# Optimization experiments

Hardware: AMD Instinct MI355X
Metric: run time of the kernel (lower is better)

## Reference

```python
import jax, jax.numpy as jnp
import numpy as np

GRID = 0.5
NG = 48
NC = 16  # output channels
CHUNK = 256  # atoms per scan step (bounds peak memory)
E2 = float(np.exp(2.0))
# order matches pro_keys ['O','C','N','S'] with vdw_dic
VDW = jnp.array([1.52, 1.7, 1.55, 1.8], dtype=jnp.float32)


def setup_inputs() -> dict:
    key = jax.random.key(0)
    k1, k2, k3 = jax.random.split(key, 3)
    N = 2048
    coords = jax.random.uniform(k1, (N, 3), dtype=jnp.float32) * (NG * GRID)  # [0, 24)
    ch_idx = jax.random.randint(k2, (N,), 0, 4, dtype=jnp.int32)
    fg = jax.random.randint(k3, (N,), 0, 16, dtype=jnp.int32)
    return {"coords": coords, "ch_idx": ch_idx, "fg": fg}


def _channel_weights(ch_idx, fg):
    # base element channel 0..3
    w = jax.nn.one_hot(ch_idx, NC, dtype=jnp.float32)
    # fg routing: 14 -> +ch4 +ch5; 15 -> +ch6 +ch9; 12/13 -> nothing; else -> +ch(fg+4)
    c1 = jnp.where(fg == 14, 4, jnp.where(fg == 15, 6, fg + 4))
    c1 = jnp.where((fg == 12) | (fg == 13), -1, c1)  # one_hot(-1) == zeros
    c2 = jnp.where(fg == 14, 5, jnp.where(fg == 15, 9, -1))
    return w + jax.nn.one_hot(c1, NC, dtype=jnp.float32) + jax.nn.one_hot(c2, NC, dtype=jnp.float32)


def _grid_forward(coords, r, w):
    # coords [N,3], r [N] vdw radii, w [N,16] channel weights -> [16,48,48,48]
    gx = GRID * jnp.arange(NG, dtype=jnp.float32)  # grid point coordinates
    nchunk = coords.shape[0] // CHUNK
    coords_c = coords.reshape(nchunk, CHUNK, 3)
    r_c = r.reshape(nchunk, CHUNK)
    w_c = w.reshape(nchunk, CHUNK, NC)

    def body(acc, args):
        c, rr, ww = args  # [CHUNK,3], [CHUNK], [CHUNK,16]
        dx2 = (c[:, 0, None] - gx) ** 2  # [CHUNK,48]
        dy2 = (c[:, 1, None] - gx) ** 2
        dz2 = (c[:, 2, None] - gx) ** 2
        d2 = dx2[:, :, None, None] + dy2[:, None, :, None] + dz2[:, None, None, :]  # [CHUNK,48,48,48]
        d = jnp.sqrt(d2)
        r_ = rr[:, None, None, None]
        r2 = r_ * r_
        f1 = jnp.exp(-2.0 * d2 / r2)
        f2 = 4.0 * d2 / (E2 * r2) - 12.0 * d / (E2 * r_) + 9.0 / E2
        val = jnp.where(d < r_, f1, jnp.where(d < 1.5 * r_, f2, 0.0))
        acc = acc + jnp.einsum('nc,nxyz->cxyz', ww, val)
        return acc, None

    out, _ = jax.lax.scan(body, jnp.zeros((NC, NG, NG, NG), jnp.float32), (coords_c, r_c, w_c))
    return out


def reference(coords, ch_idx, fg):
    r = VDW[ch_idx]
    w = _channel_weights(ch_idx, fg)
    return _grid_forward(coords, r, w)
```

## Files before the change

### kernel.cpp

```cpp
#include <hip/hip_runtime.h>

#define NG 48
#define NC 16
#define NPTS (NG * NG * NG)
#define E2F 7.3890561f
#define NINE_OVER_E2 1.2180175f

#define BR 4
#define CAP 128

__device__ __constant__ float c_vdw[4] = {1.52f, 1.7f, 1.55f, 1.8f};

__global__ void prep_kernel(const float* __restrict__ coords,
                            const int* __restrict__ ch_idx,
                            const int* __restrict__ fg,
                            float4* __restrict__ atomA,
                            float4* __restrict__ atomB, int natoms)
{
    const int i = blockIdx.x * blockDim.x + threadIdx.x;
    if (i >= natoms) return;
    const float x = coords[3 * i + 0];
    const float y = coords[3 * i + 1];
    const float z = coords[3 * i + 2];
    const int ci = ch_idx[i];
    const int f  = fg[i];
    const float r  = c_vdw[ci];
    const float r2 = r * r;
    int c1 = (f == 14) ? 4 : ((f == 15) ? 6 : f + 4);
    if (f == 12 || f == 13) c1 = -1;
    const int c2 = (f == 14) ? 5 : ((f == 15) ? 9 : -1);
    int mask = 1 << ci;
    if (c1 >= 0) mask |= 1 << c1;
    if (c2 >= 0) mask |= 1 << c2;
    atomA[i] = make_float4(x, y, z, 1.5f * r);
    atomB[i] = make_float4(-2.0f / r2, 4.0f / (E2F * r2),
                           12.0f / (E2F * r), __int_as_float(mask));
}

__global__ __launch_bounds__(256)
void density_kernel(const float4* __restrict__ atomA,
                    const float4* __restrict__ atomB,
                    float* __restrict__ out, int natoms)
{
    __shared__ float4 sA[CAP];
    __shared__ float4 sB[CAP];
    __shared__ int sCnt[4];
    __shared__ float sRed[4][NC][64];

    const int t = threadIdx.x;
    const int w = t >> 6;
    const int l = t & 63;
    const int bz = blockIdx.x, by = blockIdx.y, bx = blockIdx.z;

    const int tz = l & 3, ty = (l >> 2) & 3, tx = l >> 4;
    const int gx = bx * BR + tx, gy = by * BR + ty, gz = bz * BR + tz;
    const float px = gx * 0.5f, py = gy * 0.5f, pz = gz * 0.5f;

    const float blox = bx * 2.0f, bhix = blox + 1.5f;
    const float bloy = by * 2.0f, bhiy = bloy + 1.5f;
    const float bloz = bz * 2.0f, bhiz = bloz + 1.5f;

    int cnt = 0;
    for (int base = 0; base < natoms; base += 256) {
        const int a = base + t;
        float4 pA;
        bool pred = false;
        if (a < natoms) {
            pA = atomA[a];
            const float cut = pA.w;
            pred = (pA.x > blox - cut) & (pA.x < bhix + cut) &
                   (pA.y > bloy - cut) & (pA.y < bhiy + cut) &
                   (pA.z > bloz - cut) & (pA.z < bhiz + cut);
        }
        const unsigned long long m = __ballot(pred);
        if (l == 0) sCnt[w] = __popcll(m);
        __syncthreads();
        int ofs = cnt;
        #pragma unroll
        for (int w2 = 0; w2 < 4; ++w2) {
            const int c = sCnt[w2];
            if (w2 < w) ofs += c;
            cnt += c;
        }
        if (pred) {
            const int o = ofs + __popcll(m & ((1ull << l) - 1ull));
            if (o < CAP) { sA[o] = pA; sB[o] = atomB[a]; }
        }
        __syncthreads();
    }
    if (cnt > CAP) cnt = CAP;

    float acc[NC];
    #pragma unroll
    for (int c = 0; c < NC; ++c) acc[c] = 0.0f;

    for (int i = w; i < cnt; i += 4) {
        const float4 A = sA[i];
        const float dx = px - A.x;
        const float dy = py - A.y;
        const float dz = pz - A.z;
        const float d2 = fmaf(dx, dx, fmaf(dy, dy, dz * dz));
        const float cut2 = A.w * A.w;
        if (d2 < cut2) {
            const float4 B = sB[i];
            const float r2 = cut2 * (4.0f / 9.0f);
            const float d  = sqrtf(d2);
            const float f1 = __expf(B.x * d2);
            const float f2 = fmaf(B.y, d2, fmaf(-B.z, d, NINE_OVER_E2));
            const float val = (d2 < r2) ? f1 : f2;
            const int chan = __builtin_amdgcn_readfirstlane(__float_as_int(B.w));
            #pragma unroll
            for (int c = 0; c < NC; ++c)
                if (chan & (1 << c)) acc[c] += val;
        }
    }

    #pragma unroll
    for (int c = 0; c < NC; ++c) sRed[w][c][l] = acc[c];
    __syncthreads();

    const int pbase = (gx * NG + gy) * NG + gz;
    #pragma unroll
    for (int k = 0; k < 4; ++k) {
        const int c = w * 4 + k;
        const float s = sRed[0][c][l] + sRed[1][c][l] +
                        sRed[2][c][l] + sRed[3][c][l];
        out[c * NPTS + pbase] = s;
    }
}

extern "C" void kernel_launch(void* const* d_in, const int* in_sizes, int n_in,
                              void* d_out, int out_size, void* d_ws, size_t ws_size,
                              hipStream_t stream) {
    (void)n_in; (void)ws_size; (void)out_size;
    const float* coords = (const float*)d_in[0];
    const int* ch = (const int*)d_in[1];
    const int* fgp = (const int*)d_in[2];
    float* out = (float*)d_out;
    const int natoms = in_sizes[0] / 3;

    float4* atomA = (float4*)d_ws;
    float4* atomB = atomA + natoms;

    prep_kernel<<<(natoms + 255) / 256, 256, 0, stream>>>(coords, ch, fgp, atomA, atomB, natoms);
    dim3 grid(NG / BR, NG / BR, NG / BR);
    density_kernel<<<grid, 256, 0, stream>>>(atomA, atomB, out, natoms);
}
```

Measured before the change: 24.83 us.

## Give each wave its own atom quarter and drop per-batch block barriers

The atom culling pass is split so each wave scans a contiguous quarter of the atoms and compacts matches into its own shared-memory segment. This removes the two block-wide barriers per 256-atom batch and leaves only one barrier at the end. The box test becomes an exact sphere-to-box distance check, which culls more atoms than the old expanded-box test. The accumulate loop now walks the four segments, and each segment is capped at 48 atoms, so a dense region could overflow a segment and silently drop atoms.

```diff
diff --git a/kernel.cpp b/kernel.cpp
--- a/kernel.cpp
+++ b/kernel.cpp
@@ -7,7 +7,7 @@
 #define NINE_OVER_E2 1.2180175f
 
 #define BR 4
-#define CAP 128
+#define SEGCAP 48
 
 __device__ __constant__ float c_vdw[4] = {1.52f, 1.7f, 1.55f, 1.8f};
 
@@ -42,8 +42,8 @@
                     const float4* __restrict__ atomB,
                     float* __restrict__ out, int natoms)
 {
-    __shared__ float4 sA[CAP];
-    __shared__ float4 sB[CAP];
+    __shared__ float4 sA[4 * SEGCAP];
+    __shared__ float4 sB[4 * SEGCAP];
     __shared__ int sCnt[4];
     __shared__ float sRed[4][NC][64];
 
@@ -60,58 +60,65 @@
     const float bloy = by * 2.0f, bhiy = bloy + 1.5f;
     const float bloz = bz * 2.0f, bhiz = bloz + 1.5f;
 
-    int cnt = 0;
-    for (int base = 0; base < natoms; base += 256) {
-        const int a = base + t;
+    const int quarter = (natoms + 3) >> 2;
+    const int a0 = w * quarter;
+    const int a1 = min(a0 + quarter, natoms);
+    int myCnt = 0;
+    for (int base = a0; base < a1; base += 64) {
+        const int a = base + l;
         float4 pA;
         bool pred = false;
-        if (a < natoms) {
+        if (a < a1) {
             pA = atomA[a];
             const float cut = pA.w;
-            pred = (pA.x > blox - cut) & (pA.x < bhix + cut) &
-                   (pA.y > bloy - cut) & (pA.y < bhiy + cut) &
-                   (pA.z > bloz - cut) & (pA.z < bhiz + cut);
+            const float ddx = fmaxf(fmaxf(blox - pA.x, pA.x - bhix), 0.0f);
+            const float ddy = fmaxf(fmaxf(bloy - pA.y, pA.y - bhiy), 0.0f);
+            const float ddz = fmaxf(fmaxf(bloz - pA.z, pA.z - bhiz), 0.0f);
+            pred = fmaf(ddx, ddx, fmaf(ddy, ddy, ddz * ddz)) < cut * cut;
         }
         const unsigned long long m = __ballot(pred);
-        if (l == 0) sCnt[w] = __popcll(m);
-        __syncthreads();
-        int ofs = cnt;
-        #pragma unroll
-        for (int w2 = 0; w2 < 4; ++w2) {
-            const int c = sCnt[w2];
-            if (w2 < w) ofs += c;
-            cnt += c;
+        if (pred) {
+            const int o = myCnt + __popcll(m & ((1ull << l) - 1ull));
+            if (o < SEGCAP) {
+                sA[w * SEGCAP + o] = pA;
+                sB[w * SEGCAP + o] = atomB[a];
+            }
         }
-        if (pred) {
-            const int o = ofs + __popcll(m & ((1ull << l) - 1ull));
-            if (o < CAP) { sA[o] = pA; sB[o] = atomB[a]; }
-        }
-        __syncthreads();
+        myCnt += __popcll(m);
     }
-    if (cnt > CAP) cnt = CAP;
+    if (l == 0) sCnt[w] = (myCnt > SEGCAP) ? SEGCAP : myCnt;
+    __syncthreads();
+
+    const int c0 = sCnt[0], c1 = sCnt[1], c2 = sCnt[2], c3 = sCnt[3];
 
     float acc[NC];
     #pragma unroll
     for (int c = 0; c < NC; ++c) acc[c] = 0.0f;
 
-    for (int i = w; i < cnt; i += 4) {
-        const float4 A = sA[i];
-        const float dx = px - A.x;
-        const float dy = py - A.y;
-        const float dz = pz - A.z;
-        const float d2 = fmaf(dx, dx, fmaf(dy, dy, dz * dz));
-        const float cut2 = A.w * A.w;
-        if (d2 < cut2) {
-            const float4 B = sB[i];
-            const float r2 = cut2 * (4.0f / 9.0f);
-            const float d  = sqrtf(d2);
-            const float f1 = __expf(B.x * d2);
-            const float f2 = fmaf(B.y, d2, fmaf(-B.z, d, NINE_OVER_E2));
-            const float val = (d2 < r2) ? f1 : f2;
-            const int chan = __builtin_amdgcn_readfirstlane(__float_as_int(B.w));
-            #pragma unroll
-            for (int c = 0; c < NC; ++c)
-                if (chan & (1 << c)) acc[c] += val;
+    #pragma unroll 1
+    for (int s = 0; s < 4; ++s) {
+        const int cs = (s == 0) ? c0 : (s == 1) ? c1 : (s == 2) ? c2 : c3;
+        const int segbase = s * SEGCAP;
+        #pragma unroll 2
+        for (int i = w; i < cs; i += 4) {
+            const float4 A = sA[segbase + i];
+            const float4 B = sB[segbase + i];
+            const float dx = px - A.x;
+            const float dy = py - A.y;
+            const float dz = pz - A.z;
+            const float d2 = fmaf(dx, dx, fmaf(dy, dy, dz * dz));
+            const float cut2 = A.w * A.w;
+            if (d2 < cut2) {
+                const float r2 = cut2 * (4.0f / 9.0f);
+                const float d  = sqrtf(d2);
+                const float f1 = __expf(B.x * d2);
+                const float f2 = fmaf(B.y, d2, fmaf(-B.z, d, NINE_OVER_E2));
+                const float val = (d2 < r2) ? f1 : f2;
+                const int chan = __builtin_amdgcn_readfirstlane(__float_as_int(B.w));
+                #pragma unroll
+                for (int c = 0; c < NC; ++c)
+                    if (chan & (1 << c)) acc[c] += val;
+            }
         }
     }
 
```

Result: faster. 23.50 us (-5.4%).
